# Kernel optimization log

Measured on AMD Instinct MI355X. Metric: run time of the kernel, lower is better.

Reference implementation:

```python
import jax, jax.numpy as jnp
import numpy as np

S, N, H = 4096, 32, 512

def setup_inputs() -> dict:
    key = jax.random.key(0)
    ks = jax.random.split(key, 8)
    scale = 1.0 / np.sqrt(H)
    return {
        "hidden": jax.random.normal(ks[0], (N, H), dtype=jnp.float32),
        "encoder_outputs": jax.random.normal(ks[1], (S, N, H), dtype=jnp.float32),
        "W_w": jax.random.uniform(ks[2], (H, H), jnp.float32, -scale, scale),
        "W_b": jax.random.uniform(ks[3], (H,), jnp.float32, -scale, scale),
        "U_w": jax.random.uniform(ks[4], (H, H), jnp.float32, -scale, scale),
        "U_b": jax.random.uniform(ks[5], (H,), jnp.float32, -scale, scale),
        "v_w": jax.random.uniform(ks[6], (1, H), jnp.float32, -scale, scale),
        "v_b": jax.random.uniform(ks[7], (1,), jnp.float32, -scale, scale),
    }

def reference(hidden, encoder_outputs, W_w, W_b, U_w, U_b, v_w, v_b):
    # W(hidden): [N,H] -> broadcast over seq dim (equivalent to expand then Linear)
    wh = hidden @ W_w.T + W_b                      # [N, H]
    ue = jnp.einsum('snh,kh->snk', encoder_outputs, U_w) + U_b  # [S, N, H]
    energy = jnp.tanh(wh[None, :, :] + ue)         # [S, N, H]
    score = jnp.einsum('snh,oh->sno', energy, v_w) + v_b        # [S, N, 1]
    attention_weights = jax.nn.softmax(score, axis=0)           # softmax over seq
    context = jnp.sum(attention_weights * encoder_outputs, axis=0)  # [N, H]
    return (context, attention_weights)
```

## Files before the change

### kernel.cpp

```cpp
#include <hip/hip_runtime.h>
#include <hip/hip_bf16.h>

#define Sdim 4096
#define Ndim 32
#define Hdim 512
#define Mdim (Sdim * Ndim)

#define BM 128
#define BN 256
#define BK 64

typedef __bf16 bf16x8 __attribute__((ext_vector_type(8)));
typedef float f32x4 __attribute__((ext_vector_type(4)));
typedef unsigned short ushort8v __attribute__((ext_vector_type(8)));

__device__ __forceinline__ void load_lds16(const void* g, void* l) {
    __builtin_amdgcn_global_load_lds(
        (const __attribute__((address_space(1))) void*)g,
        (__attribute__((address_space(3))) void*)l, 16, 0, 0);
}

__device__ __forceinline__ float ftanh(float x) {
    float e = __expf(2.f * x);
    return 1.f - 2.f / (e + 1.f);
}

__global__ __launch_bounds__(256) void k_prep(
    const float* __restrict__ hidden, const float* __restrict__ Ww,
    const float* __restrict__ Wb, const float* __restrict__ Ubias,
    float* __restrict__ bias, const float* __restrict__ Uw,
    unsigned short* __restrict__ Ub16) {
    const int t = threadIdx.x;
    if (blockIdx.x < 128) {
        const int w = t >> 6, lane = t & 63;
        const int cc = blockIdx.x * 4 + w;
        const float4 w0 = *(const float4*)(Ww + (size_t)cc * Hdim + lane * 8);
        const float4 w1 =
            *(const float4*)(Ww + (size_t)cc * Hdim + lane * 8 + 4);
        const float wb = Wb[cc] + Ubias[cc];
        for (int n = 0; n < Ndim; ++n) {
            const float4 h0 = *(const float4*)(hidden + n * Hdim + lane * 8);
            const float4 h1 =
                *(const float4*)(hidden + n * Hdim + lane * 8 + 4);
            float p = w0.x * h0.x + w0.y * h0.y + w0.z * h0.z + w0.w * h0.w +
                      w1.x * h1.x + w1.y * h1.y + w1.z * h1.z + w1.w * h1.w;
            p += __shfl_xor(p, 1);  p += __shfl_xor(p, 2);
            p += __shfl_xor(p, 4);  p += __shfl_xor(p, 8);
            p += __shfl_xor(p, 16); p += __shfl_xor(p, 32);
            if (lane == 0) bias[n * Hdim + cc] = p + wb;
        }
    } else {
        const int i = (blockIdx.x - 128) * 256 + t;
        float4 v = ((const float4*)Uw)[i];
        union { __hip_bfloat162 h[2]; ushort4 u; } r;
        r.h[0] = __float22bfloat162_rn(make_float2(v.x, v.y));
        r.h[1] = __float22bfloat162_rn(make_float2(v.z, v.w));
        ((ushort4*)Ub16)[i] = r.u;
    }
}

__global__ __launch_bounds__(512, 4) void k_gemm_score(
    const float* __restrict__ enc,
    const unsigned short* __restrict__ Ub,
    const float* __restrict__ bias,
    const float* __restrict__ vw,
    float* __restrict__ scorep) {
    __shared__ __align__(16) unsigned short Asm[BM][72];
    __shared__ __align__(16) unsigned short Bsm[BN * BK];
    __shared__ float ssm[4][BM];

    const int t = threadIdx.x;
    const int lane = t & 63;
    const int w = t >> 6;
    const int wM = w >> 2;
    const int wN = w & 3;
    const int c = lane & 15;
    const int q = lane >> 4;

    const int rowblk = blockIdx.x >> 1;
    const int colblk = blockIdx.x & 1;
    const int mBase = rowblk * BM;
    const int colBase = colblk * BN;

    const int ar = t >> 2;
    const int aq = t & 3;
    const int asw = ((ar >> 3) & 1) << 1;
    const float4* arow =
        (const float4*)(enc + (size_t)(mBase + ar) * Hdim) + aq * 4;
    unsigned short* awr = &Asm[ar][((2 * aq) ^ asw) * 8];

    const int coff = lane >> 3;
    const int bch = (lane & 7) ^ coff;
    const unsigned short* bsrc =
        Ub + (size_t)(colBase + w * 8 + coff) * Hdim + bch * 8;
    unsigned short* bdst = Bsm + (w * 8) * BK;

    const int sA = ((c >> 3) & 1) << 1;
    const int sB = c & 7;

    f32x4 acc[4][4];
#pragma unroll
    for (int i = 0; i < 4; ++i)
#pragma unroll
        for (int j = 0; j < 4; ++j) acc[i][j] = (f32x4){0.f, 0.f, 0.f, 0.f};

    float4 a0 = *(const float4*)(arow + 0);
    float4 a1 = *(const float4*)(arow + 1);
    float4 a2 = *(const float4*)(arow + 2);
    float4 a3 = *(const float4*)(arow + 3);

#pragma unroll 1
    for (int kk = 0; kk < Hdim / BK; ++kk) {
        asm volatile("" ::: "memory");
        __builtin_amdgcn_s_barrier();
        asm volatile("" ::: "memory");
        __builtin_amdgcn_sched_barrier(0);

#pragma unroll
        for (int g = 0; g < 4; ++g)
            load_lds16(bsrc + (size_t)g * 64 * Hdim + kk * BK,
                       bdst + g * 64 * BK);
        asm volatile("" ::: "memory");
        __builtin_amdgcn_sched_barrier(0);

        union { __hip_bfloat162 h[4]; ushort8v v; } p0, p1;
        p0.h[0] = __float22bfloat162_rn(make_float2(a0.x, a0.y));
        p0.h[1] = __float22bfloat162_rn(make_float2(a0.z, a0.w));
        p0.h[2] = __float22bfloat162_rn(make_float2(a1.x, a1.y));
        p0.h[3] = __float22bfloat162_rn(make_float2(a1.z, a1.w));
        p1.h[0] = __float22bfloat162_rn(make_float2(a2.x, a2.y));
        p1.h[1] = __float22bfloat162_rn(make_float2(a2.z, a2.w));
        p1.h[2] = __float22bfloat162_rn(make_float2(a3.x, a3.y));
        p1.h[3] = __float22bfloat162_rn(make_float2(a3.z, a3.w));
        *(ushort8v*)awr = p0.v;
        *(ushort8v*)(awr + 8) = p1.v;

        const int kn = (kk < Hdim / BK - 1) ? kk + 1 : kk;
        const float4* ap = arow + kn * 16;
        a0 = ap[0]; a1 = ap[1]; a2 = ap[2]; a3 = ap[3];

        asm volatile("" ::: "memory");
        __builtin_amdgcn_sched_barrier(0);
        asm volatile("s_waitcnt vmcnt(4) lgkmcnt(0)" ::: "memory");
        __builtin_amdgcn_s_barrier();
        asm volatile("" ::: "memory");
        __builtin_amdgcn_sched_barrier(0);

#pragma unroll 1
        for (int h = 0; h < 2; ++h) {
            bf16x8 af[4], bfr[4];
#pragma unroll
            for (int mi = 0; mi < 4; ++mi) {
                const int row = wM * 64 + mi * 16 + c;
                af[mi] =
                    *(const bf16x8*)&Asm[row][(((h << 2) | q) ^ sA) * 8];
            }
#pragma unroll
            for (int ni = 0; ni < 4; ++ni) {
                const int lc = wN * 64 + ni * 16 + c;
                bfr[ni] = *(const bf16x8*)&Bsm[lc * BK +
                                               (((h << 2) | q) ^ sB) * 8];
            }
#pragma unroll
            for (int mi = 0; mi < 4; ++mi)
#pragma unroll
                for (int ni = 0; ni < 4; ++ni)
                    acc[mi][ni] = __builtin_amdgcn_mfma_f32_16x16x32_bf16(
                        af[mi], bfr[ni], acc[mi][ni], 0, 0, 0);
        }
    }
    asm volatile("" :: "v"(a0.x), "v"(a1.x), "v"(a2.x), "v"(a3.x));

    float vcol[4];
#pragma unroll
    for (int ni = 0; ni < 4; ++ni)
        vcol[ni] = vw[colBase + wN * 64 + ni * 16 + c];

#pragma unroll
    for (int mi = 0; mi < 4; ++mi) {
#pragma unroll
        for (int reg = 0; reg < 4; ++reg) {
            const int rl = wM * 64 + mi * 16 + q * 4 + reg;
            const int n = rl & 31;
            float p = 0.f;
#pragma unroll
            for (int ni = 0; ni < 4; ++ni) {
                const int col = colBase + wN * 64 + ni * 16 + c;
                float e = acc[mi][ni][reg] + bias[n * Hdim + col];
                p += vcol[ni] * ftanh(e);
            }
            p += __shfl_xor(p, 1);
            p += __shfl_xor(p, 2);
            p += __shfl_xor(p, 4);
            p += __shfl_xor(p, 8);
            if (c == 0) ssm[wN][rl] = p;
        }
    }
    __syncthreads();
    if (t < BM) {
        const int m = mBase + t;
        const float s = ssm[0][t] + ssm[1][t] + ssm[2][t] + ssm[3][t];
        scorep[colblk * Mdim + (m & 31) * Sdim + (m >> 5)] = s;
    }
}

__global__ __launch_bounds__(256) void k_sumexp(
    const float* __restrict__ scorep,
    float* __restrict__ sums) {
    const int n = blockIdx.x;
    const int t = threadIdx.x;
    const int w = t >> 6;
    const float4* p0 = (const float4*)(scorep + n * Sdim);
    const float4* p1 = (const float4*)(scorep + Mdim + n * Sdim);
    float s = 0.f;
    for (int i = t; i < Sdim / 4; i += 256) {
        const float4 a = p0[i], b = p1[i];
        s += __expf(a.x + b.x) + __expf(a.y + b.y) + __expf(a.z + b.z) +
             __expf(a.w + b.w);
    }
#pragma unroll
    for (int o = 32; o > 0; o >>= 1) s += __shfl_xor(s, o);
    __shared__ float red[4];
    if ((t & 63) == 0) red[w] = s;
    __syncthreads();
    if (t == 0) sums[n] = 1.f / (red[0] + red[1] + red[2] + red[3]);
}

__global__ __launch_bounds__(512) void k_context(
    const float* __restrict__ enc, const float* __restrict__ scorep,
    const float* __restrict__ sums, float* __restrict__ out_w,
    float* __restrict__ part) {
    const int n = blockIdx.x & 31;
    const int sc = blockIdx.x >> 5;
    const int s0 = sc * 128;
    const int t = threadIdx.x;
    const int g = t >> 6;
    const int lane = t & 63;
    const int h0 = lane * 8;

    __shared__ float wsm[128];
    if (t < 128) {
        const int s = s0 + t;
        const float sv = scorep[n * Sdim + s] + scorep[Mdim + n * Sdim + s];
        const float wv = __expf(sv) * sums[n];
        wsm[t] = wv;
        out_w[(size_t)s * Ndim + n] = wv;
    }
    __syncthreads();

    float4 c0 = {0.f, 0.f, 0.f, 0.f}, c1 = {0.f, 0.f, 0.f, 0.f};
#pragma unroll 4
    for (int it = 0; it < 16; ++it) {
        const int s = s0 + it * 8 + g;
        const float wv = wsm[it * 8 + g];
        const float* e = enc + ((size_t)s * Ndim + n) * Hdim + h0;
        const float4 e0 = *(const float4*)e;
        const float4 e1 = *(const float4*)(e + 4);
        c0.x += wv * e0.x; c0.y += wv * e0.y;
        c0.z += wv * e0.z; c0.w += wv * e0.w;
        c1.x += wv * e1.x; c1.y += wv * e1.y;
        c1.z += wv * e1.z; c1.w += wv * e1.w;
    }
    __shared__ __align__(16) float4 red[7][128];
    if (g > 0) { red[g - 1][lane * 2] = c0; red[g - 1][lane * 2 + 1] = c1; }
    __syncthreads();
    if (g == 0) {
#pragma unroll
        for (int i = 0; i < 7; ++i) {
            const float4 b0 = red[i][lane * 2];
            const float4 b1 = red[i][lane * 2 + 1];
            c0.x += b0.x; c0.y += b0.y; c0.z += b0.z; c0.w += b0.w;
            c1.x += b1.x; c1.y += b1.y; c1.z += b1.z; c1.w += b1.w;
        }
        float* o = part + (size_t)(sc * 32 + n) * Hdim + h0;
        *(float4*)o = c0;
        *(float4*)(o + 4) = c1;
    }
}

__global__ __launch_bounds__(256) void k_ctx_reduce(
    const float* __restrict__ part, float* __restrict__ out) {
    const int j = blockIdx.x * 256 + threadIdx.x;
    float4 s = {0.f, 0.f, 0.f, 0.f};
    for (int i = 0; i < 32; ++i) {
        const float4 v = ((const float4*)part)[i * 4096 + j];
        s.x += v.x; s.y += v.y; s.z += v.z; s.w += v.w;
    }
    ((float4*)out)[j] = s;
}

extern "C" void kernel_launch(void* const* d_in, const int* in_sizes, int n_in,
                              void* d_out, int out_size, void* d_ws,
                              size_t ws_size, hipStream_t stream) {
    const float* hidden = (const float*)d_in[0];
    const float* enc    = (const float*)d_in[1];
    const float* Ww     = (const float*)d_in[2];
    const float* Wb     = (const float*)d_in[3];
    const float* Uw     = (const float*)d_in[4];
    const float* Ubias  = (const float*)d_in[5];
    const float* vw     = (const float*)d_in[6];

    float* out = (float*)d_out;

    char* ws = (char*)d_ws;
    float* bias          = (float*)(ws);
    unsigned short* Ub16 = (unsigned short*)(ws + (64 << 10));
    float* scorep        = (float*)(ws + (576 << 10));
    float* sums          = (float*)(ws + (1600 << 10));
    float* part          = (float*)(ws + (1664 << 10));

    k_prep<<<384, 256, 0, stream>>>(hidden, Ww, Wb, Ubias, bias, Uw, Ub16);
    k_gemm_score<<<(Mdim / BM) * 2, 512, 0, stream>>>(enc, Ub16, bias, vw,
                                                      scorep);
    k_sumexp<<<Ndim, 256, 0, stream>>>(scorep, sums);
    k_context<<<Ndim * (Sdim / 128), 512, 0, stream>>>(enc, scorep, sums,
                                                       out + Ndim * Hdim, part);
    k_ctx_reduce<<<16, 256, 0, stream>>>(part, out);
}
```

Before: 483.6 us.

## Swizzle GEMM block order and restructure context reduction over contiguous seq rows

The GEMM grid index is remapped so the two column tiles of nearby row tiles are scheduled close together, aiming for better cache reuse of the encoder rows. The context kernel now assigns each block a contiguous range of 16 sequence positions across all batches and hidden units, reading fully contiguous rows and dropping the intra-block LDS reduction. This produces 256 partial buffers instead of 32, so the final reduce kernel reads more partial data. The larger workspace footprint and fewer context blocks trade occupancy for contiguous access.

```diff
diff --git a/kernel.cpp b/kernel.cpp
--- a/kernel.cpp
+++ b/kernel.cpp
@@ -9,6 +9,9 @@
 #define BM 128
 #define BN 256
 #define BK 64
+
+#define SC 256
+#define SCR (Sdim / SC)
 
 typedef __bf16 bf16x8 __attribute__((ext_vector_type(8)));
 typedef float f32x4 __attribute__((ext_vector_type(4)));
@@ -77,8 +80,9 @@
     const int c = lane & 15;
     const int q = lane >> 4;
 
-    const int rowblk = blockIdx.x >> 1;
-    const int colblk = blockIdx.x & 1;
+    const int x = blockIdx.x;
+    const int rowblk = (x & 7) | ((x >> 4) << 3);
+    const int colblk = (x >> 3) & 1;
     const int mBase = rowblk * BM;
     const int colBase = colblk * BN;
 
@@ -230,17 +234,14 @@
     const float* __restrict__ enc, const float* __restrict__ scorep,
     const float* __restrict__ sums, float* __restrict__ out_w,
     float* __restrict__ part) {
-    const int n = blockIdx.x & 31;
-    const int sc = blockIdx.x >> 5;
-    const int s0 = sc * 128;
-    const int t = threadIdx.x;
-    const int g = t >> 6;
-    const int lane = t & 63;
-    const int h0 = lane * 8;
-
-    __shared__ float wsm[128];
-    if (t < 128) {
-        const int s = s0 + t;
+    const int sc = blockIdx.x;
+    const int s0 = sc * SCR;
+    const int t = threadIdx.x;
+
+    __shared__ float wsm[SCR * Ndim];
+    {
+        const int sl = t >> 5, n = t & 31;
+        const int s = s0 + sl;
         const float sv = scorep[n * Sdim + s] + scorep[Mdim + n * Sdim + s];
         const float wv = __expf(sv) * sums[n];
         wsm[t] = wv;
@@ -248,45 +249,55 @@
     }
     __syncthreads();
 
-    float4 c0 = {0.f, 0.f, 0.f, 0.f}, c1 = {0.f, 0.f, 0.f, 0.f};
-#pragma unroll 4
-    for (int it = 0; it < 16; ++it) {
-        const int s = s0 + it * 8 + g;
-        const float wv = wsm[it * 8 + g];
-        const float* e = enc + ((size_t)s * Ndim + n) * Hdim + h0;
-        const float4 e0 = *(const float4*)e;
-        const float4 e1 = *(const float4*)(e + 4);
-        c0.x += wv * e0.x; c0.y += wv * e0.y;
-        c0.z += wv * e0.z; c0.w += wv * e0.w;
-        c1.x += wv * e1.x; c1.y += wv * e1.y;
-        c1.z += wv * e1.z; c1.w += wv * e1.w;
-    }
-    __shared__ __align__(16) float4 red[7][128];
-    if (g > 0) { red[g - 1][lane * 2] = c0; red[g - 1][lane * 2 + 1] = c1; }
-    __syncthreads();
-    if (g == 0) {
-#pragma unroll
-        for (int i = 0; i < 7; ++i) {
-            const float4 b0 = red[i][lane * 2];
-            const float4 b1 = red[i][lane * 2 + 1];
-            c0.x += b0.x; c0.y += b0.y; c0.z += b0.z; c0.w += b0.w;
-            c1.x += b1.x; c1.y += b1.y; c1.z += b1.z; c1.w += b1.w;
+    float4 acc[8];
+#pragma unroll
+    for (int j = 0; j < 8; ++j) acc[j] = (float4){0.f, 0.f, 0.f, 0.f};
+
+#pragma unroll 2
+    for (int s = 0; s < SCR; ++s) {
+        const float4* row =
+            (const float4*)enc + (size_t)(s0 + s) * (Ndim * Hdim / 4);
+#pragma unroll
+        for (int j = 0; j < 8; ++j) {
+            const int idx = t + j * 512;
+            const float wv = wsm[s * 32 + (idx >> 7)];
+            const float4 e = row[idx];
+            acc[j].x += wv * e.x; acc[j].y += wv * e.y;
+            acc[j].z += wv * e.z; acc[j].w += wv * e.w;
         }
-        float* o = part + (size_t)(sc * 32 + n) * Hdim + h0;
-        *(float4*)o = c0;
-        *(float4*)(o + 4) = c1;
-    }
+    }
+    float4* po = (float4*)part + (size_t)sc * 4096;
+#pragma unroll
+    for (int j = 0; j < 8; ++j) po[t + j * 512] = acc[j];
 }
 
 __global__ __launch_bounds__(256) void k_ctx_reduce(
     const float* __restrict__ part, float* __restrict__ out) {
-    const int j = blockIdx.x * 256 + threadIdx.x;
+    const int b = blockIdx.x;
+    const int t = threadIdx.x;
+    const int isub = t >> 6;
+    const int jo = t & 63;
+    const int j4 = b * 64 + jo;
+    const float4* p = (const float4*)part;
     float4 s = {0.f, 0.f, 0.f, 0.f};
-    for (int i = 0; i < 32; ++i) {
-        const float4 v = ((const float4*)part)[i * 4096 + j];
+#pragma unroll 4
+    for (int i = isub; i < SC; i += 4) {
+        const float4 v = p[(size_t)i * 4096 + j4];
         s.x += v.x; s.y += v.y; s.z += v.z; s.w += v.w;
     }
-    ((float4*)out)[j] = s;
+    __shared__ __align__(16) float4 red[4][64];
+    red[isub][jo] = s;
+    __syncthreads();
+    if (t < 64) {
+        const float4 a = red[0][t], c = red[1][t], d = red[2][t],
+                     e = red[3][t];
+        float4 r;
+        r.x = a.x + c.x + d.x + e.x;
+        r.y = a.y + c.y + d.y + e.y;
+        r.z = a.z + c.z + d.z + e.z;
+        r.w = a.w + c.w + d.w + e.w;
+        ((float4*)out)[b * 64 + t] = r;
+    }
 }
 
 extern "C" void kernel_launch(void* const* d_in, const int* in_sizes, int n_in,
@@ -313,7 +324,7 @@
     k_gemm_score<<<(Mdim / BM) * 2, 512, 0, stream>>>(enc, Ub16, bias, vw,
                                                       scorep);
     k_sumexp<<<Ndim, 256, 0, stream>>>(scorep, sums);
-    k_context<<<Ndim * (Sdim / 128), 512, 0, stream>>>(enc, scorep, sums,
-                                                       out + Ndim * Hdim, part);
-    k_ctx_reduce<<<16, 256, 0, stream>>>(part, out);
-}
+    k_context<<<SC, 512, 0, stream>>>(enc, scorep, sums, out + Ndim * Hdim,
+                                      part);
+    k_ctx_reduce<<<64, 256, 0, stream>>>(part, out);
+}
```

Measured after the change: 487.5 us. No clear change (+0.8%).
